# Kernel tuning notes

Measured on AMD Instinct MI355X. Metric: run time of the kernel, lower is better.

## Reference

```python
import jax, jax.numpy as jnp
import numpy as np

B, T, D_IN, H, D = 4, 4096, 1024, 16, 64


def setup_inputs() -> dict:
    key = jax.random.key(0)
    k1, k2, k3 = jax.random.split(key, 3)
    inputs = jax.random.normal(k1, (B, T, D_IN), dtype=jnp.float32)
    kv_kernel = jax.random.normal(k2, (D_IN, H, D, 2), dtype=jnp.float32) * (1.0 / np.sqrt(D_IN))
    q_kernel = jax.random.normal(k3, (H, D), dtype=jnp.float32) * (1.0 / np.sqrt(D))
    return {"inputs": inputs, "kv_kernel": kv_kernel, "q_kernel": q_kernel}


def _associate(a, b):
    # Online-softmax combine on packed tuples [m(1), u(1), w(D)] along last axis.
    ma, ua, wa = a[..., :1], a[..., 1:2], a[..., 2:]
    mb, ub, wb = b[..., :1], b[..., 1:2], b[..., 2:]
    m = jnp.maximum(ma, mb)
    ea = jnp.exp(ma - m)
    eb = jnp.exp(mb - m)
    u = ua * ea + ub * eb
    w = wa * ea + wb * eb
    return jnp.concatenate([m, u, w], axis=-1)


def reference(inputs, kv_kernel, q_kernel):
    # inputs: (B,T,D_in); kv_kernel: (D_in,H,D,2); q_kernel: (H,D)
    kv = jnp.einsum('bti,ihdk->bthdk', inputs, kv_kernel)
    kv = jax.nn.relu(kv)  # activation; dropout disabled (inference)
    k = kv[..., 0]  # (B,T,H,D)
    v = kv[..., 1]  # (B,T,H,D)
    st = jnp.einsum('hd,bthd->bth', q_kernel, k)[..., None]  # (B,T,H,1)
    u_init = jnp.ones_like(st)  # exp(s - m) with m = s
    elems = jnp.concatenate([st, u_init, v], axis=-1)  # (B,T,H,D+2)
    o = jax.lax.associative_scan(_associate, elems, axis=1)
    c = o[..., 1:2]  # running denominator
    a = o[..., 2:]   # running numerator (B,T,H,D)
    h = a / c
    # concat_heads=False -> sum over heads
    return jnp.sum(h, axis=-2)  # (B,T,D)
```

## Files before the change

kernel.cpp:

```cpp
#include <hip/hip_runtime.h>
#include <hip/hip_bf16.h>
#include <math.h>

#define B_   4
#define T_   4096
#define DIN_ 1024
#define H_   16
#define D_   64
#define M_   (B_*T_)
#define N_   (H_*D_*2)
#define K_   DIN_
#define C_   64
#define CL_  (T_/C_)

typedef unsigned short u16;
typedef __attribute__((ext_vector_type(8))) short short8_t;
typedef __attribute__((ext_vector_type(4))) float float4_t;

__device__ __forceinline__ u16 f2bf(float f) {
  unsigned int x = __float_as_uint(f);
  x += 0x7fffu + ((x >> 16) & 1u);
  return (u16)(x >> 16);
}
__device__ __forceinline__ float bf2f(unsigned int u) {
  return __uint_as_float((u & 0xffffu) << 16);
}

__device__ __forceinline__ void g2l16(const u16* g, u16* l) {
  __builtin_amdgcn_global_load_lds(
      (const __attribute__((address_space(1))) void*)g,
      (__attribute__((address_space(3))) void*)l, 16, 0, 0);
}

__global__ __launch_bounds__(256)
void prep(const float* __restrict__ inputs, const float* __restrict__ kvk,
          u16* __restrict__ aB, u16* __restrict__ wBt) {
  __shared__ float tile[32][33];
  int bid = blockIdx.x;
  int tid = threadIdx.x;
  if (bid < 8192) {
    int i = bid * 256 + tid;
    const float4* src = (const float4*)inputs;
    float4 a = src[2*i], b = src[2*i+1];
    uint4 o;
    o.x = (unsigned)f2bf(a.x) | ((unsigned)f2bf(a.y) << 16);
    o.y = (unsigned)f2bf(a.z) | ((unsigned)f2bf(a.w) << 16);
    o.z = (unsigned)f2bf(b.x) | ((unsigned)f2bf(b.y) << 16);
    o.w = (unsigned)f2bf(b.z) | ((unsigned)f2bf(b.w) << 16);
    ((uint4*)aB)[i] = o;
  } else {
    int b2 = bid - 8192;
    int kb = (b2 & 31) * 32;
    int nb = (b2 >> 5) * 32;
    int r  = tid >> 3;
    int c4 = (tid & 7) * 4;
    float4 v = *(const float4*)&kvk[(size_t)(kb + r) * N_ + nb + c4];
    tile[r][c4+0] = v.x; tile[r][c4+1] = v.y; tile[r][c4+2] = v.z; tile[r][c4+3] = v.w;
    __syncthreads();
    unsigned lo = (unsigned)f2bf(tile[c4+0][r]) | ((unsigned)f2bf(tile[c4+1][r]) << 16);
    unsigned hi = (unsigned)f2bf(tile[c4+2][r]) | ((unsigned)f2bf(tile[c4+3][r]) << 16);
    uint2 o; o.x = lo; o.y = hi;
    *(uint2*)&wBt[(size_t)(nb + r) * K_ + kb + c4] = o;
  }
}

__global__ __launch_bounds__(256)
void gemm_kv(const u16* __restrict__ A, const u16* __restrict__ Bt,
             const float* __restrict__ q,
             float* __restrict__ sbuf, u16* __restrict__ vbuf,
             float* __restrict__ aggM, float* __restrict__ aggU,
             float* __restrict__ aggW) {
  __shared__ __align__(16) char smem[33536];
  u16*   lA    = (u16*)smem;
  u16*   lB    = (u16*)(smem + 16384);
  u16*   vtile = (u16*)smem;
  float* sred  = (float*)(smem + 18432);
  float* qs    = (float*)(smem + 32768);
  float* sS    = (float*)(smem + 33024);

  const int tid  = threadIdx.x;
  const int wave = tid >> 6;
  const int lane = tid & 63;
  const int quad = lane >> 4;
  const int l16  = lane & 15;

  const int g    = blockIdx.x;
  const int xcd  = g & 7;
  const int slot = g >> 3;
  const int h    = slot & 15;
  const int mt   = (slot >> 4) * 8 + xcd;
  const int bm = mt * 128;
  const int bn = h * 128;
  const int wm = (wave >> 1) * 64;
  const int wn = (wave & 1) * 64;

  if (tid < D_) qs[tid] = q[h * D_ + tid];

  const int r8 = lane >> 3;
  const int k8 = lane & 7;
  const int gk = (k8 ^ r8) * 8;
  const u16* gaBase = A  + (size_t)(bm + wave*32 + r8) * K_ + gk;
  const u16* gbBase = Bt + (size_t)(bn + wave*32 + r8) * K_ + gk;

  const int fs0 = ((quad    ) ^ (l16 & 7)) * 8;
  const int fs1 = ((quad + 4) ^ (l16 & 7)) * 8;

  float4_t acc[4][4] = {};

  for (int k0 = 0; k0 < K_; k0 += 64) {
    __syncthreads();
#pragma unroll
    for (int call = 0; call < 4; ++call) {
      g2l16(gaBase + k0 + (size_t)(call*8) * K_, lA + (wave*32 + call*8) * 64);
      g2l16(gbBase + k0 + (size_t)(call*8) * K_, lB + (wave*32 + call*8) * 64);
    }
    __syncthreads();

    short8_t af[4][2], bfr[4][2];
#pragma unroll
    for (int i = 0; i < 4; ++i) {
      int row = (wm + i*16 + l16) * 64;
      af[i][0] = *(const short8_t*)&lA[row + fs0];
      af[i][1] = *(const short8_t*)&lA[row + fs1];
    }
#pragma unroll
    for (int j = 0; j < 4; ++j) {
      int row = (wn + j*16 + l16) * 64;
      bfr[j][0] = *(const short8_t*)&lB[row + fs0];
      bfr[j][1] = *(const short8_t*)&lB[row + fs1];
    }
#pragma unroll
    for (int t = 0; t < 2; ++t)
#pragma unroll
      for (int i = 0; i < 4; ++i)
#pragma unroll
        for (int j = 0; j < 4; ++j)
          acc[i][j] = __builtin_amdgcn_mfma_f32_16x16x32_bf16(af[i][t], bfr[j][t], acc[i][j], 0, 0, 0);
  }

  __syncthreads();

  if (l16 & 1) {
#pragma unroll
    for (int j = 0; j < 4; ++j) {
      int d = ((wn + j*16 + l16) & 127) >> 1;
#pragma unroll
      for (int i = 0; i < 4; ++i)
#pragma unroll
        for (int r = 0; r < 4; ++r) {
          int t = wm + i*16 + quad*4 + r;
          vtile[t*72 + d] = f2bf(fmaxf(acc[i][j][r], 0.f));
        }
    }
  } else {
    int slot2 = (wn >> 3) + (l16 >> 1);
#pragma unroll
    for (int i = 0; i < 4; ++i)
#pragma unroll
      for (int r = 0; r < 4; ++r) {
        int t = wm + i*16 + quad*4 + r;
        float p = 0.f;
#pragma unroll
        for (int j = 0; j < 4; ++j) {
          int d = ((wn + j*16 + l16) & 127) >> 1;
          p += qs[d] * fmaxf(acc[i][j][r], 0.f);
        }
        sred[t*17 + slot2] = p;
      }
  }
  __syncthreads();

  const int b   = mt >> 5;
  const int tt0 = (mt & 31) * 128;
  const int bh  = b * H_ + h;

  if (tid < 128) {
    float ssum = 0.f;
#pragma unroll
    for (int k = 0; k < 16; ++k) ssum += sred[tid*17 + k];
    sS[tid] = ssum;
    sbuf[(size_t)bh * T_ + tt0 + tid] = ssum;
  }
  __syncthreads();

  if (wave < 2) {
    int d = lane;
    float m = -INFINITY, u = 0.f, w = 0.f;
#pragma unroll 4
    for (int i = 0; i < CL_; ++i) {
      int t = wave * CL_ + i;
      float si = sS[t];
      float v  = bf2f(vtile[t*72 + d]);
      float mn    = fmaxf(m, si);
      float alpha = __expf(m - mn);
      float p     = __expf(si - mn);
      u = u * alpha + p;
      w = w * alpha + p * v;
      m = mn;
    }
    int blk = bh * C_ + (mt & 31) * 2 + wave;
    aggW[(size_t)blk * D_ + d] = w;
    if (d == 0) { aggM[blk] = m; aggU[blk] = u; }
  } else {
    int idx = tid - 128;
    int d0  = (idx & 7) * 8;
    int tr  = idx >> 3;
    u16* vg = vbuf + ((size_t)bh * T_ + tt0) * D_;
#pragma unroll
    for (int itv = 0; itv < 8; ++itv) {
      int t = tr + 16*itv;
      uint4 val = *(const uint4*)&vtile[t*72 + d0];
      *(uint4*)&vg[(size_t)t * D_ + d0] = val;
    }
  }
}

__global__ __launch_bounds__(1024)
void scan_pass3(const u16* __restrict__ vbuf, const float* __restrict__ sbuf,
                const float* __restrict__ aggM, const float* __restrict__ aggU,
                const float* __restrict__ aggW, float* __restrict__ out) {
  __shared__ float sS[H_][CL_];
  __shared__ float wbuf[H_][8][D_ + 1];
  int bc = blockIdx.x;
  int b  = bc >> 6;
  int c  = bc & (C_ - 1);
  int tid  = threadIdx.x;
  int h    = tid >> 6;
  int lane = tid & 63;
  int bh   = b * H_ + h;
  int t0   = c * CL_;

  sS[h][lane] = sbuf[(size_t)bh * T_ + t0 + lane];

  float m = -INFINITY, u = 0.f, w = 0.f;
  for (int j = 0; j < c; ++j) {
    int idx = bh * C_ + j;
    float Mc = aggM[idx];
    float Uc = aggU[idx];
    float Wc = aggW[(size_t)idx * D_ + lane];
    float mn = fmaxf(m, Mc);
    float ea = __expf(m - mn);
    float eb = __expf(Mc - mn);
    u = u * ea + Uc * eb;
    w = w * ea + Wc * eb;
    m = mn;
  }
  __syncthreads();

  const u16* vp = vbuf + ((size_t)bh * T_ + t0) * D_ + lane;
  for (int gg = 0; gg < 8; ++gg) {
#pragma unroll
    for (int ii = 0; ii < 8; ++ii) {
      int i = gg * 8 + ii;
      float si = sS[h][i];
      float v  = bf2f(vp[i * D_]);
      float mn    = fmaxf(m, si);
      float alpha = __expf(m - mn);
      float p     = __expf(si - mn);
      u = u * alpha + p;
      w = w * alpha + p * v;
      m = mn;
      wbuf[h][ii][lane] = __fdividef(w, u);
    }
    __syncthreads();
    if (tid < 512) {
      int ii = tid >> 6, dd = tid & 63;
      float acc = 0.f;
#pragma unroll
      for (int hh = 0; hh < H_; ++hh) acc += wbuf[hh][ii][dd];
      out[((size_t)b * T_ + t0 + gg*8 + ii) * D_ + dd] = acc;
    }
    __syncthreads();
  }
}

extern "C" void kernel_launch(void* const* d_in, const int* in_sizes, int n_in,
                              void* d_out, int out_size, void* d_ws, size_t ws_size,
                              hipStream_t stream) {
  const float* inputs = (const float*)d_in[0];
  const float* kvk    = (const float*)d_in[1];
  const float* qk     = (const float*)d_in[2];
  float* out = (float*)d_out;
  char* ws = (char*)d_ws;

  u16*   aB   = (u16*)ws;
  u16*   wBt  = (u16*)(ws + 33554432);
  u16*   vb   = (u16*)(ws + 37748736);
  float* sb   = (float*)(ws + 71303168);
  float* aggM = (float*)(ws + 72351744);
  float* aggU = (float*)(ws + 72368128);
  float* aggW = (float*)(ws + 72384512);

  prep<<<10240, 256, 0, stream>>>(inputs, kvk, aB, wBt);
  gemm_kv<<<2048, 256, 0, stream>>>(aB, wBt, qk, sb, vb, aggM, aggU, aggW);
  scan_pass3<<<B_*C_, 1024, 0, stream>>>(vb, sb, aggM, aggU, aggW, out);
}
```

Baseline: 228.5 us.

## Load GEMM MFMA fragments directly from global memory instead of LDS staging

Removes the LDS-staged global_load_lds tiling in the KV GEMM and has each wave read its A/B fragments directly from global memory with vector loads. This eliminates the two barriers per K step and shrinks shared memory to just the epilogue buffers. In exchange, operand tiles are no longer shared across waves through LDS, so global/L2 traffic roughly doubles and loads are not double-buffered.

```diff
diff --git a/kernel.cpp b/kernel.cpp
--- a/kernel.cpp
+++ b/kernel.cpp
@@ -24,12 +24,6 @@
 }
 __device__ __forceinline__ float bf2f(unsigned int u) {
   return __uint_as_float((u & 0xffffu) << 16);
-}
-
-__device__ __forceinline__ void g2l16(const u16* g, u16* l) {
-  __builtin_amdgcn_global_load_lds(
-      (const __attribute__((address_space(1))) void*)g,
-      (__attribute__((address_space(3))) void*)l, 16, 0, 0);
 }
 
 __global__ __launch_bounds__(256)
@@ -70,13 +64,10 @@
              float* __restrict__ sbuf, u16* __restrict__ vbuf,
              float* __restrict__ aggM, float* __restrict__ aggU,
              float* __restrict__ aggW) {
-  __shared__ __align__(16) char smem[33536];
-  u16*   lA    = (u16*)smem;
-  u16*   lB    = (u16*)(smem + 16384);
-  u16*   vtile = (u16*)smem;
-  float* sred  = (float*)(smem + 18432);
-  float* qs    = (float*)(smem + 32768);
-  float* sS    = (float*)(smem + 33024);
+  __shared__ u16  vtile[128][72];
+  __shared__ float sred[128][17];
+  __shared__ float qs[D_];
+  __shared__ float sS[128];
 
   const int tid  = threadIdx.x;
   const int wave = tid >> 6;
@@ -96,38 +87,28 @@
 
   if (tid < D_) qs[tid] = q[h * D_ + tid];
 
-  const int r8 = lane >> 3;
-  const int k8 = lane & 7;
-  const int gk = (k8 ^ r8) * 8;
-  const u16* gaBase = A  + (size_t)(bm + wave*32 + r8) * K_ + gk;
-  const u16* gbBase = Bt + (size_t)(bn + wave*32 + r8) * K_ + gk;
-
-  const int fs0 = ((quad    ) ^ (l16 & 7)) * 8;
-  const int fs1 = ((quad + 4) ^ (l16 & 7)) * 8;
+  const u16* aP[4];
+  const u16* bP[4];
+#pragma unroll
+  for (int i = 0; i < 4; ++i)
+    aP[i] = A + (size_t)(bm + wm + i*16 + l16) * K_ + quad*8;
+#pragma unroll
+  for (int j = 0; j < 4; ++j)
+    bP[j] = Bt + (size_t)(bn + wn + j*16 + l16) * K_ + quad*8;
 
   float4_t acc[4][4] = {};
 
-  for (int k0 = 0; k0 < K_; k0 += 64) {
-    __syncthreads();
-#pragma unroll
-    for (int call = 0; call < 4; ++call) {
-      g2l16(gaBase + k0 + (size_t)(call*8) * K_, lA + (wave*32 + call*8) * 64);
-      g2l16(gbBase + k0 + (size_t)(call*8) * K_, lB + (wave*32 + call*8) * 64);
-    }
-    __syncthreads();
-
+  for (int it = 0; it < 16; ++it) {
     short8_t af[4][2], bfr[4][2];
 #pragma unroll
     for (int i = 0; i < 4; ++i) {
-      int row = (wm + i*16 + l16) * 64;
-      af[i][0] = *(const short8_t*)&lA[row + fs0];
-      af[i][1] = *(const short8_t*)&lA[row + fs1];
+      af[i][0] = *(const short8_t*)(aP[i]);
+      af[i][1] = *(const short8_t*)(aP[i] + 32);
     }
 #pragma unroll
     for (int j = 0; j < 4; ++j) {
-      int row = (wn + j*16 + l16) * 64;
-      bfr[j][0] = *(const short8_t*)&lB[row + fs0];
-      bfr[j][1] = *(const short8_t*)&lB[row + fs1];
+      bfr[j][0] = *(const short8_t*)(bP[j]);
+      bfr[j][1] = *(const short8_t*)(bP[j] + 32);
     }
 #pragma unroll
     for (int t = 0; t < 2; ++t)
@@ -136,9 +117,11 @@
 #pragma unroll
         for (int j = 0; j < 4; ++j)
           acc[i][j] = __builtin_amdgcn_mfma_f32_16x16x32_bf16(af[i][t], bfr[j][t], acc[i][j], 0, 0, 0);
-  }
-
-  __syncthreads();
+#pragma unroll
+    for (int i = 0; i < 4; ++i) aP[i] += 64;
+#pragma unroll
+    for (int j = 0; j < 4; ++j) bP[j] += 64;
+  }
 
   if (l16 & 1) {
 #pragma unroll
@@ -149,7 +132,7 @@
 #pragma unroll
         for (int r = 0; r < 4; ++r) {
           int t = wm + i*16 + quad*4 + r;
-          vtile[t*72 + d] = f2bf(fmaxf(acc[i][j][r], 0.f));
+          vtile[t][d] = f2bf(fmaxf(acc[i][j][r], 0.f));
         }
     }
   } else {
@@ -165,7 +148,7 @@
           int d = ((wn + j*16 + l16) & 127) >> 1;
           p += qs[d] * fmaxf(acc[i][j][r], 0.f);
         }
-        sred[t*17 + slot2] = p;
+        sred[t][slot2] = p;
       }
   }
   __syncthreads();
@@ -177,7 +160,7 @@
   if (tid < 128) {
     float ssum = 0.f;
 #pragma unroll
-    for (int k = 0; k < 16; ++k) ssum += sred[tid*17 + k];
+    for (int k = 0; k < 16; ++k) ssum += sred[tid][k];
     sS[tid] = ssum;
     sbuf[(size_t)bh * T_ + tt0 + tid] = ssum;
   }
@@ -190,7 +173,7 @@
     for (int i = 0; i < CL_; ++i) {
       int t = wave * CL_ + i;
       float si = sS[t];
-      float v  = bf2f(vtile[t*72 + d]);
+      float v  = bf2f(vtile[t][d]);
       float mn    = fmaxf(m, si);
       float alpha = __expf(m - mn);
       float p     = __expf(si - mn);
@@ -209,7 +192,7 @@
 #pragma unroll
     for (int itv = 0; itv < 8; ++itv) {
       int t = tr + 16*itv;
-      uint4 val = *(const uint4*)&vtile[t*72 + d0];
+      uint4 val = *(const uint4*)&vtile[t][d0];
       *(uint4*)&vg[(size_t)t * D_ + d0] = val;
     }
   }
```

After: 374.0 us. 1.64x slower.

## Fuse fp32-to-bf16 input conversion into GEMM A-tile loads with register prefetch

Applied to the files above, without the earlier changes.

Drops the separate pass that converts the activation matrix to bf16 in workspace. The GEMM now reads fp32 activations directly into registers, prefetches the next K-slice while the current one is computed, converts to bf16 and writes into swizzled LDS. This removes one write and one read of a 32 MB intermediate. In exchange, each GEMM block reads twice as many bytes for A, and the 16 head tiles per row block each reload and reconvert the same fp32 rows. Register pressure also rises because of the prefetch buffer.

```diff
diff --git a/kernel.cpp b/kernel.cpp
--- a/kernel.cpp
+++ b/kernel.cpp
@@ -25,6 +25,12 @@
 __device__ __forceinline__ float bf2f(unsigned int u) {
   return __uint_as_float((u & 0xffffu) << 16);
 }
+__device__ __forceinline__ unsigned pk_bf16(float x, float y) {
+  float2 f; f.x = x; f.y = y;
+  union { __hip_bfloat162 h2; unsigned u; } c;
+  c.h2 = __float22bfloat162_rn(f);
+  return c.u;
+}
 
 __device__ __forceinline__ void g2l16(const u16* g, u16* l) {
   __builtin_amdgcn_global_load_lds(
@@ -33,39 +39,25 @@
 }
 
 __global__ __launch_bounds__(256)
-void prep(const float* __restrict__ inputs, const float* __restrict__ kvk,
-          u16* __restrict__ aB, u16* __restrict__ wBt) {
+void prep(const float* __restrict__ kvk, u16* __restrict__ wBt) {
   __shared__ float tile[32][33];
   int bid = blockIdx.x;
   int tid = threadIdx.x;
-  if (bid < 8192) {
-    int i = bid * 256 + tid;
-    const float4* src = (const float4*)inputs;
-    float4 a = src[2*i], b = src[2*i+1];
-    uint4 o;
-    o.x = (unsigned)f2bf(a.x) | ((unsigned)f2bf(a.y) << 16);
-    o.y = (unsigned)f2bf(a.z) | ((unsigned)f2bf(a.w) << 16);
-    o.z = (unsigned)f2bf(b.x) | ((unsigned)f2bf(b.y) << 16);
-    o.w = (unsigned)f2bf(b.z) | ((unsigned)f2bf(b.w) << 16);
-    ((uint4*)aB)[i] = o;
-  } else {
-    int b2 = bid - 8192;
-    int kb = (b2 & 31) * 32;
-    int nb = (b2 >> 5) * 32;
-    int r  = tid >> 3;
-    int c4 = (tid & 7) * 4;
-    float4 v = *(const float4*)&kvk[(size_t)(kb + r) * N_ + nb + c4];
-    tile[r][c4+0] = v.x; tile[r][c4+1] = v.y; tile[r][c4+2] = v.z; tile[r][c4+3] = v.w;
-    __syncthreads();
-    unsigned lo = (unsigned)f2bf(tile[c4+0][r]) | ((unsigned)f2bf(tile[c4+1][r]) << 16);
-    unsigned hi = (unsigned)f2bf(tile[c4+2][r]) | ((unsigned)f2bf(tile[c4+3][r]) << 16);
-    uint2 o; o.x = lo; o.y = hi;
-    *(uint2*)&wBt[(size_t)(nb + r) * K_ + kb + c4] = o;
-  }
+  int kb = (bid & 31) * 32;
+  int nb = (bid >> 5) * 32;
+  int r  = tid >> 3;
+  int c4 = (tid & 7) * 4;
+  float4 v = *(const float4*)&kvk[(size_t)(kb + r) * N_ + nb + c4];
+  tile[r][c4+0] = v.x; tile[r][c4+1] = v.y; tile[r][c4+2] = v.z; tile[r][c4+3] = v.w;
+  __syncthreads();
+  uint2 o;
+  o.x = pk_bf16(tile[c4+0][r], tile[c4+1][r]);
+  o.y = pk_bf16(tile[c4+2][r], tile[c4+3][r]);
+  *(uint2*)&wBt[(size_t)(nb + r) * K_ + kb + c4] = o;
 }
 
 __global__ __launch_bounds__(256)
-void gemm_kv(const u16* __restrict__ A, const u16* __restrict__ Bt,
+void gemm_kv(const float* __restrict__ A32, const u16* __restrict__ Bt,
              const float* __restrict__ q,
              float* __restrict__ sbuf, u16* __restrict__ vbuf,
              float* __restrict__ aggM, float* __restrict__ aggU,
@@ -96,10 +88,16 @@
 
   if (tid < D_) qs[tid] = q[h * D_ + tid];
 
+  const int ar   = tid >> 4;
+  const int akp  = tid & 15;
+  const int ach  = akp >> 1;
+  const int asub = akp & 1;
+  const float* aGp = A32 + (size_t)(bm + ar) * K_ + ach*8 + asub*4;
+  const int aLp = ar*64 + ((ach ^ (ar & 7)) * 8) + asub*4;
+
   const int r8 = lane >> 3;
   const int k8 = lane & 7;
   const int gk = (k8 ^ r8) * 8;
-  const u16* gaBase = A  + (size_t)(bm + wave*32 + r8) * K_ + gk;
   const u16* gbBase = Bt + (size_t)(bn + wave*32 + r8) * K_ + gk;
 
   const int fs0 = ((quad    ) ^ (l16 & 7)) * 8;
@@ -107,12 +105,29 @@
 
   float4_t acc[4][4] = {};
 
-  for (int k0 = 0; k0 < K_; k0 += 64) {
+  float4 aReg[8];
+#pragma unroll
+  for (int s = 0; s < 8; ++s)
+    aReg[s] = *(const float4*)(aGp + (size_t)s * 16 * K_);
+
+  for (int it = 0; it < 16; ++it) {
+    const int k0 = it * 64;
     __syncthreads();
 #pragma unroll
-    for (int call = 0; call < 4; ++call) {
-      g2l16(gaBase + k0 + (size_t)(call*8) * K_, lA + (wave*32 + call*8) * 64);
+    for (int s = 0; s < 8; ++s) {
+      float4 av = aReg[s];
+      uint2 o;
+      o.x = pk_bf16(av.x, av.y);
+      o.y = pk_bf16(av.z, av.w);
+      *(uint2*)&lA[s*1024 + aLp] = o;
+    }
+#pragma unroll
+    for (int call = 0; call < 4; ++call)
       g2l16(gbBase + k0 + (size_t)(call*8) * K_, lB + (wave*32 + call*8) * 64);
+    if (it < 15) {
+#pragma unroll
+      for (int s = 0; s < 8; ++s)
+        aReg[s] = *(const float4*)(aGp + (size_t)s * 16 * K_ + k0 + 64);
     }
     __syncthreads();
 
@@ -283,15 +298,14 @@
   float* out = (float*)d_out;
   char* ws = (char*)d_ws;
 
-  u16*   aB   = (u16*)ws;
-  u16*   wBt  = (u16*)(ws + 33554432);
-  u16*   vb   = (u16*)(ws + 37748736);
-  float* sb   = (float*)(ws + 71303168);
-  float* aggM = (float*)(ws + 72351744);
-  float* aggU = (float*)(ws + 72368128);
-  float* aggW = (float*)(ws + 72384512);
-
-  prep<<<10240, 256, 0, stream>>>(inputs, kvk, aB, wBt);
-  gemm_kv<<<2048, 256, 0, stream>>>(aB, wBt, qk, sb, vb, aggM, aggU, aggW);
+  u16*   wBt  = (u16*)ws;
+  u16*   vb   = (u16*)(ws + 4194304);
+  float* sb   = (float*)(ws + 37748736);
+  float* aggM = (float*)(ws + 38797312);
+  float* aggU = (float*)(ws + 38813696);
+  float* aggW = (float*)(ws + 38830080);
+
+  prep<<<2048, 256, 0, stream>>>(kvk, wBt);
+  gemm_kv<<<2048, 256, 0, stream>>>(inputs, wBt, qk, sb, vb, aggM, aggU, aggW);
   scan_pass3<<<B_*C_, 1024, 0, stream>>>(vb, sb, aggM, aggU, aggW, out);
 }
```

Result: slower. 253.2 us (+10.8%).
